# Kernel tuning notes

Measured on AMD Instinct MI355X. Metric: run time of the kernel, lower is better.

Reference implementation:

```python
import jax, jax.numpy as jnp
import numpy as np

D_MODEL = 1024
N_HEADS = 16
D_K = D_MODEL // N_HEADS
B, S = 2, 2048
NEG = -1.0e9


def setup_inputs() -> dict:
    key = jax.random.key(0)
    ks = jax.random.split(key, 12)
    sc = 1.0 / np.sqrt(D_MODEL)
    inp = {
        'query': jax.random.normal(ks[0], (B, S, D_MODEL), jnp.float32),
        'key': jax.random.normal(ks[1], (B, S, D_MODEL), jnp.float32),
        'value': jax.random.normal(ks[2], (B, S, D_MODEL), jnp.float32),
        # causal mask, broadcast over batch: 1 = attend, 0 = masked
        'mask': jnp.broadcast_to(jnp.tril(jnp.ones((S, S), jnp.int32)), (B, S, S)),
        'wq': jax.random.normal(ks[3], (D_MODEL, D_MODEL), jnp.float32) * sc,
        'bq': jnp.zeros((D_MODEL,), jnp.float32),
        'wk': jax.random.normal(ks[4], (D_MODEL, D_MODEL), jnp.float32) * sc,
        'bk': jnp.zeros((D_MODEL,), jnp.float32),
        'wv': jax.random.normal(ks[5], (D_MODEL, D_MODEL), jnp.float32) * sc,
        'bv': jnp.zeros((D_MODEL,), jnp.float32),
        'wo': jax.random.normal(ks[6], (D_MODEL, D_MODEL), jnp.float32) * sc,
        'bo': jnp.zeros((D_MODEL,), jnp.float32),
    }
    return inp


def reference(query, key, value, mask, wq, bq, wk, bk, wv, bv, wo, bo):
    b, sq, _ = query.shape
    sk = key.shape[1]
    # linear projections, split into heads: [B, H, S, d_k]
    def proj(x, w, bias, s):
        return (x @ w + bias).reshape(b, s, N_HEADS, D_K).transpose(0, 2, 1, 3)
    Q = proj(query, wq, bq, sq)
    K = proj(key, wk, bk, sk)
    V = proj(value, wv, bv, sk)
    # scaled dot-product attention with full score matrix [B, H, Sq, Sk]
    scores = jnp.einsum('bhqd,bhkd->bhqk', Q, K) / np.sqrt(D_K)
    scores = jnp.where(mask[:, None, :, :] == 0, NEG, scores)
    attn = jax.nn.softmax(scores, axis=-1)
    ctx = jnp.einsum('bhqk,bhkd->bhqd', attn, V)
    ctx = ctx.transpose(0, 2, 1, 3).reshape(b, sq, D_MODEL)
    return ctx @ wo + bo
```

## Files before the change

kernel.cpp:

```cpp
#include <hip/hip_runtime.h>
#include <stdint.h>

#define AS1 __attribute__((address_space(1)))
#define AS3 __attribute__((address_space(3)))

typedef __attribute__((ext_vector_type(8))) __bf16 bf16x8;
typedef __attribute__((ext_vector_type(4))) float f32x4;
typedef __attribute__((ext_vector_type(4))) unsigned int u32x4;
typedef __attribute__((ext_vector_type(2))) unsigned int u32x2;

static __device__ __forceinline__ void gload16(const void* g, void* l) {
    __builtin_amdgcn_global_load_lds((AS1 void*)(uintptr_t)g, (AS3 void*)l, 16, 0, 0);
}

static __device__ __forceinline__ unsigned cvt_pk_bf16(float lo, float hi) {
    unsigned r;
    asm volatile("v_cvt_pk_bf16_f32 %0, %1, %2" : "=v"(r) : "v"(lo), "v"(hi));
    return r;
}
static __device__ __forceinline__ unsigned short f2bf(float f) {
    return (unsigned short)(cvt_pk_bf16(f, 0.f) & 0xffffu);
}

static __device__ __forceinline__ f32x4 mfma16(bf16x8 a, bf16x8 b, f32x4 c) {
    return __builtin_amdgcn_mfma_f32_16x16x32_bf16(a, b, c, 0, 0, 0);
}

static __device__ __forceinline__ float fexp2(float x) {
    return __builtin_amdgcn_exp2f(x);
}

__global__ __launch_bounds__(256) void k_prep(
    const float* __restrict__ w0, const float* __restrict__ w1,
    const float* __restrict__ w2, const float* __restrict__ w3,
    const float* __restrict__ aq, const float* __restrict__ ak,
    const float* __restrict__ av,
    unsigned short* __restrict__ o0, unsigned short* __restrict__ o1,
    unsigned short* __restrict__ o2, unsigned short* __restrict__ o3,
    unsigned short* __restrict__ cq, unsigned short* __restrict__ ck,
    unsigned short* __restrict__ cv) {
    __shared__ unsigned short tile[64][72];
    const int tid = threadIdx.x;
    const int bid = blockIdx.x;
    if (bid < 1024) {
        const float* W;
        unsigned short* Wt;
        switch (bid >> 8) {
            case 0: W = w0; Wt = o0; break;
            case 1: W = w1; Wt = o1; break;
            case 2: W = w2; Wt = o2; break;
            default: W = w3; Wt = o3; break;
        }
        const int xy = bid & 255;
        const int k0 = (xy & 15) * 64, n0 = (xy >> 4) * 64;
#pragma unroll
        for (int j = 0; j < 4; ++j) {
            int c = j * 256 + tid;
            int kr = c >> 4, c4 = c & 15;
            f32x4 v = *(const f32x4*)(W + (size_t)(k0 + kr) * 1024 + n0 + c4 * 4);
#pragma unroll
            for (int e = 0; e < 4; ++e) tile[c4 * 4 + e][kr] = f2bf(v[e]);
        }
        __syncthreads();
#pragma unroll
        for (int j = 0; j < 2; ++j) {
            int c = j * 256 + tid;
            int nr = c >> 3, kc = c & 7;
            union { unsigned short s[8]; u32x4 v; } t;
#pragma unroll
            for (int e = 0; e < 8; ++e) t.s[e] = tile[nr][kc * 8 + e];
            *(u32x4*)(Wt + (size_t)(n0 + nr) * 1024 + k0 + kc * 8) = t.v;
        }
    } else {
        const int c = bid - 1024;
        const float* src; unsigned short* dst;
        switch (c >> 11) {
            case 0: src = aq; dst = cq; break;
            case 1: src = ak; dst = ck; break;
            default: src = av; dst = cv; break;
        }
        const size_t i = ((size_t)(c & 2047) * 256 + tid) * 8;
        f32x4 a = *(const f32x4*)(src + i);
        f32x4 b = *(const f32x4*)(src + i + 4);
        u32x4 o;
        o[0] = cvt_pk_bf16(a[0], a[1]);
        o[1] = cvt_pk_bf16(a[2], a[3]);
        o[2] = cvt_pk_bf16(b[0], b[1]);
        o[3] = cvt_pk_bf16(b[2], b[3]);
        *(u32x4*)(dst + i) = o;
    }
}

template <int OUT_F32>
static __device__ __forceinline__ void gemm128_body(
    const unsigned short* __restrict__ A, const unsigned short* __restrict__ Bt,
    const float* __restrict__ bias, void* __restrict__ Cp, float cscale,
    char* sA, char* sB) {
    const int tid = threadIdx.x;
    const int wave = tid >> 6, lane = tid & 63, g = lane >> 4, l16 = lane & 15;
    const int wm = wave & 1, wn = wave >> 1;
    const int m0 = blockIdx.x * 128, n0 = blockIdx.y * 128;
    const int K = 1024, N = 1024;

    f32x4 acc[4][4];
#pragma unroll
    for (int i = 0; i < 4; ++i)
#pragma unroll
        for (int j = 0; j < 4; ++j) acc[i][j] = (f32x4){0.f, 0.f, 0.f, 0.f};

#pragma unroll 1
    for (int kt = 0; kt < 16; ++kt) {
        const int k0 = kt << 6;
        __syncthreads();
#pragma unroll
        for (int j = 0; j < 4; ++j) {
            int c = j * 256 + tid;
            int row = c >> 3, ch = c & 7, kc = ch ^ (row & 7);
            gload16(A + (size_t)(m0 + row) * K + k0 + kc * 8, sA + c * 16);
            gload16(Bt + (size_t)(n0 + row) * K + k0 + kc * 8, sB + c * 16);
        }
        __syncthreads();
#pragma unroll
        for (int ks = 0; ks < 2; ++ks) {
            bf16x8 af[4], bfr[4];
#pragma unroll
            for (int mi = 0; mi < 4; ++mi) {
                int row = wm * 64 + mi * 16 + l16;
                int c = (ks * 4 + g) ^ (row & 7);
                af[mi] = *(const bf16x8*)(sA + row * 128 + c * 16);
            }
#pragma unroll
            for (int ni = 0; ni < 4; ++ni) {
                int row = wn * 64 + ni * 16 + l16;
                int c = (ks * 4 + g) ^ (row & 7);
                bfr[ni] = *(const bf16x8*)(sB + row * 128 + c * 16);
            }
#pragma unroll
            for (int mi = 0; mi < 4; ++mi)
#pragma unroll
                for (int ni = 0; ni < 4; ++ni)
                    acc[mi][ni] = mfma16(af[mi], bfr[ni], acc[mi][ni]);
        }
    }
#pragma unroll
    for (int ni = 0; ni < 4; ++ni) {
        int col = n0 + wn * 64 + ni * 16 + l16;
        float bn = bias[col];
#pragma unroll
        for (int mi = 0; mi < 4; ++mi) {
            int rbase = m0 + wm * 64 + mi * 16 + g * 4;
#pragma unroll
            for (int r = 0; r < 4; ++r) {
                float v = (acc[mi][ni][r] + bn) * cscale;
                if constexpr (OUT_F32)
                    ((float*)Cp)[(size_t)(rbase + r) * N + col] = v;
                else
                    ((unsigned short*)Cp)[(size_t)(rbase + r) * N + col] = f2bf(v);
            }
        }
    }
}

__global__ __launch_bounds__(256) void k_gemm_qkv(
    const unsigned short* __restrict__ Aq, const unsigned short* __restrict__ Ak,
    const unsigned short* __restrict__ Av,
    const unsigned short* __restrict__ Wq, const unsigned short* __restrict__ Wk,
    const unsigned short* __restrict__ Wv,
    const float* __restrict__ bq, const float* __restrict__ bk, const float* __restrict__ bv,
    unsigned short* __restrict__ Q2, unsigned short* __restrict__ K2,
    unsigned short* __restrict__ V2) {
    __shared__ __align__(16) char sA[16384], sB[16384];
    const unsigned short* A; const unsigned short* Bt; const float* bias;
    unsigned short* C; float sc;
    switch (blockIdx.z) {
        case 0:  A = Aq; Bt = Wq; bias = bq; C = Q2; sc = 0.18033688011112042f; break;
        case 1:  A = Ak; Bt = Wk; bias = bk; C = K2; sc = 1.0f; break;
        default: A = Av; Bt = Wv; bias = bv; C = V2; sc = 1.0f; break;
    }
    gemm128_body<0>(A, Bt, bias, C, sc, sA, sB);
}

__global__ __launch_bounds__(256) void k_gemm_o(const unsigned short* __restrict__ ctx,
                                                const unsigned short* __restrict__ Wo,
                                                const float* __restrict__ bo,
                                                float* __restrict__ out) {
    __shared__ __align__(16) char sA[16384], sB[16384];
    gemm128_body<1>(ctx, Wo, bo, out, 1.0f, sA, sB);
}

__global__ __launch_bounds__(256) void k_vtrans(const unsigned short* __restrict__ V2,
                                                unsigned short* __restrict__ Vt) {
    __shared__ unsigned short tile[64][72];
    const int tid = threadIdx.x;
    const int s0 = blockIdx.x * 64;
    const int bh = blockIdx.y, b = bh >> 4, h = bh & 15;
#pragma unroll
    for (int j = 0; j < 2; ++j) {
        int c = j * 256 + tid;
        int sr = c >> 3, dc = c & 7;
        union { u32x4 v; unsigned short s[8]; } t;
        t.v = *(const u32x4*)(V2 + (size_t)(b * 2048 + s0 + sr) * 1024 + h * 64 + dc * 8);
#pragma unroll
        for (int e = 0; e < 8; ++e) tile[dc * 8 + e][sr] = t.s[e];
    }
    __syncthreads();
#pragma unroll
    for (int j = 0; j < 2; ++j) {
        int c = j * 256 + tid;
        int dr = c >> 3, sc = c & 7;
        union { unsigned short s[8]; u32x4 v; } t;
#pragma unroll
        for (int e = 0; e < 8; ++e) t.s[e] = tile[dr][sc * 8 + e];
        *(u32x4*)(Vt + ((size_t)bh * 64 + dr) * 2048 + s0 + sc * 8) = t.v;
    }
}

__global__ __launch_bounds__(128) void k_attn(const unsigned short* __restrict__ Q2,
                                              const unsigned short* __restrict__ K2,
                                              const unsigned short* __restrict__ Vt,
                                              unsigned short* __restrict__ ctx) {
    __shared__ __align__(16) char sK[8192];
    __shared__ __align__(16) char sV[2][8192];
    __shared__ __align__(16) char sP[2][2048];

    const int tid = threadIdx.x, w = tid >> 6, lane = tid & 63;
    const int g = lane >> 4, l16 = lane & 15;
    const int bid = blockIdx.x;
    const int xcd = bid & 7, j = bid >> 3;
    const int bh = xcd * 4 + (j & 3);
    const int p = j >> 2;
    const int b = bh >> 4, h = bh & 15;
    const int swzl = (l16 & 7) << 4;

    const int r0 = tid >> 3;
    const int sc0 = (tid & 7) ^ (r0 & 7);
    const unsigned short* ksrc = K2 + (size_t)(b * 2048 + r0) * 1024 + h * 64 + sc0 * 8;
    const unsigned short* vsrc = Vt + ((size_t)bh * 64 + r0) * 2048 + sc0 * 8;
    char* const myp = sP[w];
    char* const mypw = myp + l16 * 128;

#pragma unroll 1
    for (int t2 = 0; t2 < 2; ++t2) {
        const int t = t2 ? p : (63 - p);
        const int wq0 = t * 32 + w * 16;
        const int qg = wq0 + l16;

        const unsigned short* qp = Q2 + (size_t)(b * 2048 + wq0 + l16) * 1024 + h * 64;
        bf16x8 qf0 = *(const bf16x8*)(qp + g * 8);
        bf16x8 qf1 = *(const bf16x8*)(qp + 32 + g * 8);

        f32x4 accO[4];
#pragma unroll
        for (int i = 0; i < 4; ++i) accO[i] = (f32x4){0.f, 0.f, 0.f, 0.f};
        float m = 0.f, lsum = 0.f;

        const int nkv = (t >> 1) + 1;
        const int diag = t >> 1;
        __syncthreads();
#pragma unroll
        for (int rr = 0; rr < 4; ++rr) {
            gload16(ksrc + (size_t)(rr * 16) * 1024, sK + rr * 2048 + tid * 16);
            gload16(vsrc + (size_t)(rr * 16) * 2048, sV[0] + rr * 2048 + tid * 16);
        }
        __syncthreads();

        const unsigned short* kstage = ksrc + 64 * 1024;
        const unsigned short* vstage = vsrc + 64;

#pragma unroll 1
        for (int kt = 0; kt < nkv; ++kt) {
            const int cur = kt & 1;
            const int kv0 = kt * 64;
            float s[16];
            __builtin_amdgcn_s_setprio(1);
#pragma unroll
            for (int blk = 0; blk < 4; ++blk) {
                const int rl = blk * 16 + l16;
                const char* krow = sK + rl * 128;
                bf16x8 kf0 = *(const bf16x8*)(krow + ((g << 4) ^ swzl));
                bf16x8 kf1 = *(const bf16x8*)(krow + (((4 + g) << 4) ^ swzl));
                f32x4 a = (f32x4){0.f, 0.f, 0.f, 0.f};
                a = mfma16(kf0, qf0, a);
                a = mfma16(kf1, qf1, a);
#pragma unroll
                for (int rr = 0; rr < 4; ++rr) s[blk * 4 + rr] = a[rr];
            }
            __builtin_amdgcn_s_setprio(0);
            __syncthreads();
            if (kt + 1 < nkv) {
#pragma unroll
                for (int rr = 0; rr < 4; ++rr) {
                    gload16(kstage + (size_t)(rr * 16) * 1024, sK + rr * 2048 + tid * 16);
                    gload16(vstage + (size_t)(rr * 16) * 2048, sV[cur ^ 1] + rr * 2048 + tid * 16);
                }
                kstage += 64 * 1024;
                vstage += 64;
            }
            if (kt == diag) {
#pragma unroll
                for (int j2 = 0; j2 < 16; ++j2) {
                    int kvg = kv0 + (j2 >> 2) * 16 + g * 4 + (j2 & 3);
                    if (kvg > qg) s[j2] = -1e9f;
                }
            }
            float ps0 = 0.f, ps1 = 0.f, ps2 = 0.f, ps3 = 0.f;
            unsigned pk[8];
#pragma unroll
            for (int j2 = 0; j2 < 4; ++j2) {
                float a0 = fexp2(s[4 * j2] - m);
                float a1 = fexp2(s[4 * j2 + 1] - m);
                float a2 = fexp2(s[4 * j2 + 2] - m);
                float a3 = fexp2(s[4 * j2 + 3] - m);
                ps0 += a0; ps1 += a1; ps2 += a2; ps3 += a3;
                pk[2 * j2] = cvt_pk_bf16(a0, a1);
                pk[2 * j2 + 1] = cvt_pk_bf16(a2, a3);
            }
            float ps = (ps0 + ps1) + (ps2 + ps3);
            if (__any(ps > 16777216.f)) {
                float c1 = fmaxf(fmaxf(s[0], s[1]), s[2]);
                c1 = fmaxf(fmaxf(c1, s[3]), s[4]);
                c1 = fmaxf(fmaxf(c1, s[5]), s[6]);
                c1 = fmaxf(c1, s[7]);
                float c2 = fmaxf(fmaxf(s[8], s[9]), s[10]);
                c2 = fmaxf(fmaxf(c2, s[11]), s[12]);
                c2 = fmaxf(fmaxf(c2, s[13]), s[14]);
                c2 = fmaxf(c2, s[15]);
                float mx = fmaxf(c1, c2);
                mx = fmaxf(mx, __shfl_xor(mx, 16));
                mx = fmaxf(mx, __shfl_xor(mx, 32));
                float mnew = fmaxf(m, mx);
                float scl = fexp2(m - mnew);
                lsum *= scl;
#pragma unroll
                for (int dt = 0; dt < 4; ++dt) accO[dt] = accO[dt] * scl;
                m = mnew;
                ps = 0.f;
#pragma unroll
                for (int j2 = 0; j2 < 8; ++j2) {
                    float p0 = fexp2(s[2 * j2] - m);
                    float p1 = fexp2(s[2 * j2 + 1] - m);
                    ps += p0 + p1;
                    pk[j2] = cvt_pk_bf16(p0, p1);
                }
            }
            lsum += ps;
#pragma unroll
            for (int blk = 0; blk < 4; ++blk) {
                u32x2 pw = {pk[blk * 2], pk[blk * 2 + 1]};
                *(u32x2*)(mypw + ((blk * 32 + g * 8) ^ swzl)) = pw;
            }
            __builtin_amdgcn_s_setprio(1);
#pragma unroll
            for (int kvh = 0; kvh < 2; ++kvh) {
                bf16x8 pf = *(const bf16x8*)(mypw + ((kvh * 64 + g * 16) ^ swzl));
#pragma unroll
                for (int dt = 0; dt < 4; ++dt) {
                    const int rv = dt * 16 + l16;
                    bf16x8 vf = *(const bf16x8*)(sV[cur] + rv * 128 + (((kvh * 4 + g) << 4) ^ swzl));
                    accO[dt] = mfma16(vf, pf, accO[dt]);
                }
            }
            __builtin_amdgcn_s_setprio(0);
            __syncthreads();
        }
        float v = lsum;
        v += __shfl_xor(v, 16);
        v += __shfl_xor(v, 32);
        float inv = 1.f / v;
        unsigned short* cp = ctx + (size_t)(b * 2048 + wq0 + l16) * 1024 + h * 64 + g * 4;
#pragma unroll
        for (int dt = 0; dt < 4; ++dt) {
            u32x2 o;
            o[0] = cvt_pk_bf16(accO[dt][0] * inv, accO[dt][1] * inv);
            o[1] = cvt_pk_bf16(accO[dt][2] * inv, accO[dt][3] * inv);
            *(u32x2*)(cp + dt * 16) = o;
        }
    }
}

extern "C" void kernel_launch(void* const* d_in, const int* in_sizes, int n_in,
                              void* d_out, int out_size, void* d_ws, size_t ws_size,
                              hipStream_t stream) {
    const float* query = (const float*)d_in[0];
    const float* key   = (const float*)d_in[1];
    const float* value = (const float*)d_in[2];
    const float* wq = (const float*)d_in[4];
    const float* bq = (const float*)d_in[5];
    const float* wk = (const float*)d_in[6];
    const float* bk = (const float*)d_in[7];
    const float* wv = (const float*)d_in[8];
    const float* bv = (const float*)d_in[9];
    const float* wo = (const float*)d_in[10];
    const float* bo = (const float*)d_in[11];
    float* out = (float*)d_out;

    char* ws = (char*)d_ws;
    unsigned short* Wtq = (unsigned short*)ws;
    unsigned short* Wtk = Wtq + 1024 * 1024;
    unsigned short* Wtv = Wtk + 1024 * 1024;
    unsigned short* Wto = Wtv + 1024 * 1024;
    unsigned short* Q2  = Wto + 1024 * 1024;
    unsigned short* K2  = Q2 + 4096 * 1024;
    unsigned short* V2  = K2 + 4096 * 1024;
    unsigned short* Aq  = V2 + 4096 * 1024;
    unsigned short* Ak  = Aq + 4096 * 1024;
    unsigned short* Av  = Ak + 4096 * 1024;
    unsigned short* Vt  = Aq;
    unsigned short* ctx = Ak;

    dim3 blk(256);
    k_prep<<<dim3(7168), blk, 0, stream>>>(wq, wk, wv, wo, query, key, value,
                                           Wtq, Wtk, Wtv, Wto, Aq, Ak, Av);

    k_gemm_qkv<<<dim3(32, 8, 3), blk, 0, stream>>>(Aq, Ak, Av,
                                                   Wtq, Wtk, Wtv, bq, bk, bv,
                                                   Q2, K2, V2);

    k_vtrans<<<dim3(32, 32), blk, 0, stream>>>(V2, Vt);
    k_attn<<<dim3(1024), dim3(128), 0, stream>>>(Q2, K2, Vt, ctx);

    k_gemm_o<<<dim3(32, 8), blk, 0, stream>>>(ctx, Wto, bo, out);
}
```

Before: 128.5 us.

## Double-buffer GEMM LDS staging and shrink M tile to 64

```diff
diff --git a/kernel.cpp b/kernel.cpp
--- a/kernel.cpp
+++ b/kernel.cpp
@@ -92,63 +92,81 @@
 }
 
 template <int OUT_F32>
-static __device__ __forceinline__ void gemm128_body(
-    const unsigned short* __restrict__ A, const unsigned short* __restrict__ Bt,
-    const float* __restrict__ bias, void* __restrict__ Cp, float cscale,
-    char* sA, char* sB) {
+static __device__ __forceinline__ void gemm_body(const unsigned short* __restrict__ A,
+                                                 const unsigned short* __restrict__ Bt,
+                                                 const float* __restrict__ bias,
+                                                 void* __restrict__ Cp,
+                                                 int M, int N, int K, float cscale,
+                                                 char* smem) {
+    constexpr int ASZ = 8192;
+    char* sA = smem;
+    char* sB = smem + 2 * ASZ;
     const int tid = threadIdx.x;
     const int wave = tid >> 6, lane = tid & 63, g = lane >> 4, l16 = lane & 15;
     const int wm = wave & 1, wn = wave >> 1;
-    const int m0 = blockIdx.x * 128, n0 = blockIdx.y * 128;
-    const int K = 1024, N = 1024;
-
-    f32x4 acc[4][4];
-#pragma unroll
-    for (int i = 0; i < 4; ++i)
+    const int m0 = blockIdx.x * 64, n0 = blockIdx.y * 128;
+
+    f32x4 acc[2][4];
+#pragma unroll
+    for (int i = 0; i < 2; ++i)
 #pragma unroll
         for (int j = 0; j < 4; ++j) acc[i][j] = (f32x4){0.f, 0.f, 0.f, 0.f};
 
-#pragma unroll 1
-    for (int kt = 0; kt < 16; ++kt) {
-        const int k0 = kt << 6;
-        __syncthreads();
+    auto STAGE = [&](int k0, int buf) {
+        char* dstA = sA + buf * ASZ;
+#pragma unroll
+        for (int j = 0; j < 2; ++j) {
+            int c = j * 256 + tid;
+            int row = c >> 3, w = c & 7, kc = w ^ (row & 7);
+            gload16(A + (size_t)(m0 + row) * K + k0 + kc * 8, dstA + c * 16);
+        }
+        char* dstB = sB + buf * 16384;
 #pragma unroll
         for (int j = 0; j < 4; ++j) {
             int c = j * 256 + tid;
-            int row = c >> 3, ch = c & 7, kc = ch ^ (row & 7);
-            gload16(A + (size_t)(m0 + row) * K + k0 + kc * 8, sA + c * 16);
-            gload16(Bt + (size_t)(n0 + row) * K + k0 + kc * 8, sB + c * 16);
-        }
-        __syncthreads();
+            int row = c >> 3, w = c & 7, kc = w ^ (row & 7);
+            gload16(Bt + (size_t)(n0 + row) * K + k0 + kc * 8, dstB + c * 16);
+        }
+    };
+
+    const int nkt = K >> 6;
+    STAGE(0, 0);
+    __syncthreads();
+    int cur = 0;
+#pragma unroll 1
+    for (int kt = 0; kt < nkt; ++kt) {
+        if (kt + 1 < nkt) STAGE((kt + 1) << 6, cur ^ 1);
+        const char* sAc = sA + cur * ASZ;
+        const char* sBc = sB + cur * 16384;
 #pragma unroll
         for (int ks = 0; ks < 2; ++ks) {
-            bf16x8 af[4], bfr[4];
-#pragma unroll
-            for (int mi = 0; mi < 4; ++mi) {
-                int row = wm * 64 + mi * 16 + l16;
+            bf16x8 af[2];
+#pragma unroll
+            for (int mi = 0; mi < 2; ++mi) {
+                int row = wm * 32 + mi * 16 + l16;
                 int c = (ks * 4 + g) ^ (row & 7);
-                af[mi] = *(const bf16x8*)(sA + row * 128 + c * 16);
+                af[mi] = *(const bf16x8*)(sAc + row * 128 + c * 16);
             }
 #pragma unroll
             for (int ni = 0; ni < 4; ++ni) {
                 int row = wn * 64 + ni * 16 + l16;
                 int c = (ks * 4 + g) ^ (row & 7);
-                bfr[ni] = *(const bf16x8*)(sB + row * 128 + c * 16);
-            }
-#pragma unroll
-            for (int mi = 0; mi < 4; ++mi)
-#pragma unroll
-                for (int ni = 0; ni < 4; ++ni)
-                    acc[mi][ni] = mfma16(af[mi], bfr[ni], acc[mi][ni]);
-        }
+                bf16x8 bfr = *(const bf16x8*)(sBc + row * 128 + c * 16);
+#pragma unroll
+                for (int mi = 0; mi < 2; ++mi)
+                    acc[mi][ni] = mfma16(af[mi], bfr, acc[mi][ni]);
+            }
+        }
+        __syncthreads();
+        cur ^= 1;
     }
 #pragma unroll
     for (int ni = 0; ni < 4; ++ni) {
         int col = n0 + wn * 64 + ni * 16 + l16;
         float bn = bias[col];
 #pragma unroll
-        for (int mi = 0; mi < 4; ++mi) {
-            int rbase = m0 + wm * 64 + mi * 16 + g * 4;
+        for (int mi = 0; mi < 2; ++mi) {
+            int rbase = m0 + wm * 32 + mi * 16 + g * 4;
 #pragma unroll
             for (int r = 0; r < 4; ++r) {
                 float v = (acc[mi][ni][r] + bn) * cscale;
@@ -169,7 +187,7 @@
     const float* __restrict__ bq, const float* __restrict__ bk, const float* __restrict__ bv,
     unsigned short* __restrict__ Q2, unsigned short* __restrict__ K2,
     unsigned short* __restrict__ V2) {
-    __shared__ __align__(16) char sA[16384], sB[16384];
+    extern __shared__ __align__(16) char smem[];
     const unsigned short* A; const unsigned short* Bt; const float* bias;
     unsigned short* C; float sc;
     switch (blockIdx.z) {
@@ -177,15 +195,15 @@
         case 1:  A = Ak; Bt = Wk; bias = bk; C = K2; sc = 1.0f; break;
         default: A = Av; Bt = Wv; bias = bv; C = V2; sc = 1.0f; break;
     }
-    gemm128_body<0>(A, Bt, bias, C, sc, sA, sB);
+    gemm_body<0>(A, Bt, bias, C, 4096, 1024, 1024, sc, smem);
 }
 
 __global__ __launch_bounds__(256) void k_gemm_o(const unsigned short* __restrict__ ctx,
                                                 const unsigned short* __restrict__ Wo,
                                                 const float* __restrict__ bo,
                                                 float* __restrict__ out) {
-    __shared__ __align__(16) char sA[16384], sB[16384];
-    gemm128_body<1>(ctx, Wo, bo, out, 1.0f, sA, sB);
+    extern __shared__ __align__(16) char smem[];
+    gemm_body<1>(ctx, Wo, bo, out, 4096, 1024, 1024, 1.0f, smem);
 }
 
 __global__ __launch_bounds__(256) void k_vtrans(const unsigned short* __restrict__ V2,
@@ -412,12 +430,12 @@
     k_prep<<<dim3(7168), blk, 0, stream>>>(wq, wk, wv, wo, query, key, value,
                                            Wtq, Wtk, Wtv, Wto, Aq, Ak, Av);
 
-    k_gemm_qkv<<<dim3(32, 8, 3), blk, 0, stream>>>(Aq, Ak, Av,
-                                                   Wtq, Wtk, Wtv, bq, bk, bv,
-                                                   Q2, K2, V2);
+    k_gemm_qkv<<<dim3(64, 8, 3), blk, 49152, stream>>>(Aq, Ak, Av,
+                                                       Wtq, Wtk, Wtv, bq, bk, bv,
+                                                       Q2, K2, V2);
 
     k_vtrans<<<dim3(32, 32), blk, 0, stream>>>(V2, Vt);
     k_attn<<<dim3(1024), dim3(128), 0, stream>>>(Q2, K2, Vt, ctx);
 
-    k_gemm_o<<<dim3(32, 8), blk, 0, stream>>>(ctx, Wto, bo, out);
-}
+    k_gemm_o<<<dim3(64, 8), blk, 49152, stream>>>(ctx, Wto, bo, out);
+}
```

Result: faster. 114.4 us (-11.0%).
